# Kernel tuning notes

Hardware: AMD Instinct MI355X
Metric: run time of the kernel (lower is better)

Reference implementation:

```python
import jax, jax.numpy as jnp
import numpy as np

INPUT_SIZE = 1024
OUTPUT_SIZE = 1024
BLOCK_SIZE = 60
T = 4096
EPS = 1e-12


def setup_inputs() -> dict:
    key = jax.random.key(0)
    k1, k2, k3, k4, k5 = jax.random.split(key, 5)
    s_in = 1.0 / np.sqrt(INPUT_SIZE)
    s_out = 1.0 / np.sqrt(OUTPUT_SIZE + 2)
    return {
        "x": jax.random.normal(k1, (T, INPUT_SIZE), dtype=jnp.float32),
        "Wk": jax.random.normal(k2, (OUTPUT_SIZE, INPUT_SIZE), dtype=jnp.float32) * s_in,
        "Wq": jax.random.normal(k3, (OUTPUT_SIZE, INPUT_SIZE), dtype=jnp.float32) * s_in,
        "Wv": jax.random.normal(k4, (OUTPUT_SIZE, INPUT_SIZE), dtype=jnp.float32) * s_in,
        "Wout": jax.random.normal(k5, (INPUT_SIZE, OUTPUT_SIZE + 2), dtype=jnp.float32) * s_out,
    }


def reference(x, Wk, Wq, Wv, Wout):
    t = x.shape[0]
    # L2-normalized frame similarity / diversity  [T, T]
    x_unit = x / jnp.maximum(jnp.linalg.norm(x, axis=1, keepdims=True), EPS)
    diversity = 1.0 - x_unit @ x_unit.T

    K = x @ Wk.T
    Q = x @ Wq.T
    V = x @ Wv.T
    energies = Q @ K.T                      # [T, T]
    att_weights = jax.nn.softmax(energies, axis=-1)
    logp = jax.nn.log_softmax(energies, axis=-1)
    # normalized row entropy, then L1-normalize over T (F.normalize p=1)
    entropy = -(att_weights * logp).sum(-1) / jnp.log(jnp.float32(t))
    entropy = entropy / jnp.maximum(jnp.abs(entropy).sum(), EPS)

    # block-diagonal keep mask: same block <=> same index // block_size
    blk = jnp.arange(t) // BLOCK_SIZE
    keep = (blk[:, None] == blk[None, :]).astype(att_weights.dtype)  # [T, T]
    zero = 1.0 - keep

    att_win = att_weights * keep
    attn_rem = att_weights * zero
    div_rem = diversity * zero
    dep_factor = (div_rem * attn_rem).sum(-1) / div_rem.sum(-1)      # [T]
    # dep_factor broadcast as identical rows, masked into the kept blocks
    att_win = att_win + dep_factor[None, :] * keep

    y = att_win @ V                                                   # [T, output_size]
    characteristics = jnp.stack([entropy, dep_factor])               # [2, T] (detached in torch)
    outputs = jnp.concatenate([y, characteristics.T], axis=-1)       # [T, output_size+2]
    y_out = outputs @ Wout.T                                          # [T, input_size]
    return y_out, att_win
```

## Files before the change

### kernel.cpp

```cpp
#include <hip/hip_runtime.h>
#include <math.h>

#define T_DIM 4096
#define D_DIM 1024
#define BS 60
#define NBLK 69
#define NPART 16

typedef __attribute__((ext_vector_type(4))) float f32x4;
typedef __attribute__((ext_vector_type(8))) short short8;
#define MFMAH(a,b,c) __builtin_amdgcn_mfma_f32_16x16x32_f16((a),(b),(c),0,0,0)

static __device__ __forceinline__ ushort f2h(float f) {
  _Float16 h = (_Float16)f;
  return __builtin_bit_cast(ushort, h);
}
static __device__ __forceinline__ float h2f(ushort u) {
  _Float16 h = __builtin_bit_cast(_Float16, u);
  return (float)h;
}

__global__ __launch_bounds__(256) void k_prep(const float* __restrict__ x,
    ushort* __restrict__ xhi, ushort* __restrict__ xlo, ushort* __restrict__ u) {
  int i = blockIdx.x, tid = threadIdx.x;
  size_t off = (size_t)i * D_DIM + tid * 4;
  float4 v = *reinterpret_cast<const float4*>(x + off);
  float ss = v.x*v.x + v.y*v.y + v.z*v.z + v.w*v.w;
#pragma unroll
  for (int m = 1; m < 64; m <<= 1) ss += __shfl_xor(ss, m);
  __shared__ float sb[4];
  if ((tid & 63) == 0) sb[tid >> 6] = ss;
  __syncthreads();
  float inv = 1.0f / fmaxf(sqrtf(sb[0] + sb[1] + sb[2] + sb[3]), 1e-12f);
  ushort4 h, l, un;
  h.x = f2h(v.x); l.x = f2h(v.x - h2f(h.x)); un.x = f2h(v.x*inv);
  h.y = f2h(v.y); l.y = f2h(v.y - h2f(h.y)); un.y = f2h(v.y*inv);
  h.z = f2h(v.z); l.z = f2h(v.z - h2f(h.z)); un.z = f2h(v.z*inv);
  h.w = f2h(v.w); l.w = f2h(v.w - h2f(h.w)); un.w = f2h(v.w*inv);
  *reinterpret_cast<ushort4*>(xhi + off) = h;
  *reinterpret_cast<ushort4*>(xlo + off) = l;
  *reinterpret_cast<ushort4*>(u + off) = un;
}

__global__ __launch_bounds__(256) void k_wsplit(
    const float* __restrict__ Wq, const float* __restrict__ Wk, const float* __restrict__ Wv,
    ushort* __restrict__ Wqh, ushort* __restrict__ Wkh, ushort* __restrict__ Wvh) {
  int y = blockIdx.y;
  const float* A = (y == 0) ? Wq : (y == 1) ? Wk : Wv;
  ushort* hi = (y == 0) ? Wqh : (y == 1) ? Wkh : Wvh;
  size_t i = ((size_t)blockIdx.x * 256 + threadIdx.x) * 4;
  float4 v = *reinterpret_cast<const float4*>(A + i);
  ushort4 h;
  h.x = f2h(v.x); h.y = f2h(v.y); h.z = f2h(v.z); h.w = f2h(v.w);
  *reinterpret_cast<ushort4*>(hi + i) = h;
}

__global__ __launch_bounds__(256) void k_bsum(const ushort* __restrict__ u, float* __restrict__ Sb) {
  int b = blockIdx.x, tid = threadIdx.x;
  int j0 = b * BS;
  int w = (BS < T_DIM - j0) ? BS : (T_DIM - j0);
  int c = tid * 4;
  float4 acc = {0,0,0,0};
  for (int j = 0; j < w; ++j) {
    ushort4 v = *reinterpret_cast<const ushort4*>(u + (size_t)(j0 + j) * D_DIM + c);
    acc.x += h2f(v.x); acc.y += h2f(v.y); acc.z += h2f(v.z); acc.w += h2f(v.w);
  }
  *reinterpret_cast<float4*>(Sb + (size_t)b * D_DIM + c) = acc;
}

__global__ __launch_bounds__(256) void k_gsum(const float* __restrict__ Sb, float* __restrict__ S) {
  int c = blockIdx.x * 256 + threadIdx.x;
  float s = 0.f;
  for (int b = 0; b < NBLK; ++b) s += Sb[(size_t)b * D_DIM + c];
  S[c] = s;
}

__global__ __launch_bounds__(256,2) void k_qkv(
    const ushort* __restrict__ xhi, const ushort* __restrict__ xlo,
    const ushort* __restrict__ Wqh, const ushort* __restrict__ Wkh,
    const ushort* __restrict__ Wvh,
    ushort* __restrict__ Qhi, ushort* __restrict__ Qlo,
    ushort* __restrict__ Khi, ushort* __restrict__ Vb) {
  __shared__ __align__(16) ushort lds[28672];
  const int tid = threadIdx.x;
  const int w = tid >> 6, lane = tid & 63;
  const int wr = w >> 1, wc = w & 1;
  const int g = lane >> 4, cl = lane & 15;
  const int i0 = blockIdx.y * 128, j0 = blockIdx.x * 64;

  int adA[4], adB[2];
#pragma unroll
  for (int is = 0; is < 4; ++is) {
    int r = wr*64 + is*16 + cl;
    adA[is] = r*32 + (g ^ ((r >> 1) & 3))*8;
  }
#pragma unroll
  for (int js = 0; js < 2; ++js) {
    int r = wc*32 + js*16 + cl;
    adB[js] = r*32 + (g ^ ((r >> 1) & 3))*8;
  }
  const int ra1 = tid >> 2, ra2 = 64 + (tid >> 2), rbr = tid >> 2;
  const int sa = tid & 3;
  const int wA1 = ra1*32 + (sa ^ ((ra1 >> 1) & 3))*8;
  const int wA2 = ra2*32 + (sa ^ ((ra2 >> 1) & 3))*8;
  const int wB  = rbr*32 + (sa ^ ((rbr >> 1) & 3))*8;
  const size_t gA1 = (size_t)(i0 + ra1) * D_DIM + sa*8;
  const size_t gA2 = (size_t)(i0 + ra2) * D_DIM + sa*8;
  const size_t gB  = (size_t)(j0 + rbr) * D_DIM + sa*8;

  f32x4 accQ[4][2], accK[4][2], accV[4][2];
#pragma unroll
  for (int is = 0; is < 4; ++is)
#pragma unroll
    for (int js = 0; js < 2; ++js) {
      accQ[is][js] = (f32x4){0.f,0.f,0.f,0.f};
      accK[is][js] = (f32x4){0.f,0.f,0.f,0.f};
      accV[is][js] = (f32x4){0.f,0.f,0.f,0.f};
    }

  short8 sXh1 = *reinterpret_cast<const short8*>(xhi + gA1);
  short8 sXh2 = *reinterpret_cast<const short8*>(xhi + gA2);
  short8 sXl1 = *reinterpret_cast<const short8*>(xlo + gA1);
  short8 sXl2 = *reinterpret_cast<const short8*>(xlo + gA2);
  short8 sQh  = *reinterpret_cast<const short8*>(Wqh + gB);
  short8 sKh  = *reinterpret_cast<const short8*>(Wkh + gB);
  short8 sVh  = *reinterpret_cast<const short8*>(Wvh + gB);

  for (int ks = 0; ks < 32; ++ks) {
    const int bofs = (ks & 1) * 14336;
    *reinterpret_cast<short8*>(&lds[bofs + wA1])          = sXh1;
    *reinterpret_cast<short8*>(&lds[bofs + wA2])          = sXh2;
    *reinterpret_cast<short8*>(&lds[bofs + 4096 + wA1])   = sXl1;
    *reinterpret_cast<short8*>(&lds[bofs + 4096 + wA2])   = sXl2;
    *reinterpret_cast<short8*>(&lds[bofs + 8192 + wB])    = sQh;
    *reinterpret_cast<short8*>(&lds[bofs + 10240 + wB])   = sKh;
    *reinterpret_cast<short8*>(&lds[bofs + 12288 + wB])   = sVh;
    __syncthreads();
    short8 aH[4], aL[4], bQh[2], bKh[2], bVh[2];
#pragma unroll
    for (int is = 0; is < 4; ++is) {
      aH[is] = *reinterpret_cast<const short8*>(&lds[bofs + adA[is]]);
      aL[is] = *reinterpret_cast<const short8*>(&lds[bofs + 4096 + adA[is]]);
    }
#pragma unroll
    for (int js = 0; js < 2; ++js) {
      bQh[js] = *reinterpret_cast<const short8*>(&lds[bofs + 8192  + adB[js]]);
      bKh[js] = *reinterpret_cast<const short8*>(&lds[bofs + 10240 + adB[js]]);
      bVh[js] = *reinterpret_cast<const short8*>(&lds[bofs + 12288 + adB[js]]);
    }
    if (ks < 31) {
      const int k0 = (ks + 1) * 32;
      sXh1 = *reinterpret_cast<const short8*>(xhi + gA1 + k0);
      sXh2 = *reinterpret_cast<const short8*>(xhi + gA2 + k0);
      sXl1 = *reinterpret_cast<const short8*>(xlo + gA1 + k0);
      sXl2 = *reinterpret_cast<const short8*>(xlo + gA2 + k0);
      sQh  = *reinterpret_cast<const short8*>(Wqh + gB + k0);
      sKh  = *reinterpret_cast<const short8*>(Wkh + gB + k0);
      sVh  = *reinterpret_cast<const short8*>(Wvh + gB + k0);
    }
#pragma unroll
    for (int js = 0; js < 2; ++js)
#pragma unroll
      for (int is = 0; is < 4; ++is) {
        accQ[is][js] = MFMAH(aH[is], bQh[js], accQ[is][js]);
        accQ[is][js] = MFMAH(aL[is], bQh[js], accQ[is][js]);
        accK[is][js] = MFMAH(aH[is], bKh[js], accK[is][js]);
        accK[is][js] = MFMAH(aL[is], bKh[js], accK[is][js]);
        accV[is][js] = MFMAH(aH[is], bVh[js], accV[is][js]);
      }
  }
#pragma unroll
  for (int is = 0; is < 4; ++is)
#pragma unroll
    for (int js = 0; js < 2; ++js)
#pragma unroll
      for (int a = 0; a < 4; ++a) {
        int gi = i0 + wr*64 + is*16 + g*4 + a;
        int gj = j0 + wc*32 + js*16 + cl;
        size_t o = (size_t)gi*D_DIM + gj;
        float vq = accQ[is][js][a];
        ushort hq = f2h(vq);
        Qhi[o] = hq; Qlo[o] = f2h(vq - h2f(hq));
        Khi[o] = f2h(accK[is][js][a]);
        Vb[o]  = f2h(accV[is][js][a]);
      }
}

__global__ __launch_bounds__(256,2) void k_E(
    const ushort* __restrict__ Qhi, const ushort* __restrict__ Qlo,
    const ushort* __restrict__ Khi,
    float* __restrict__ E, float* __restrict__ pm) {
  __shared__ __align__(16) ushort lds[32768];
  __shared__ float stat_s[2][2][64];
  const int tid = threadIdx.x;
  const int bid = blockIdx.x;
  const int wg = (bid & 7) * 64 + (bid >> 3);
  const int it = wg >> 4, chunk = wg & 15;
  const int i0 = it * 128, jb = chunk * 256;
  const int w = tid >> 6, lane = tid & 63;
  const int wr = w >> 1, wc = w & 1;
  const int g = lane >> 4, cl = lane & 15;

  int adA[4], adB[8];
#pragma unroll
  for (int is = 0; is < 4; ++is) {
    int r = wr*64 + is*16 + cl;
    adA[is] = r*32 + (g ^ ((r >> 1) & 3))*8;
  }
#pragma unroll
  for (int js = 0; js < 8; ++js) {
    int r = wc*128 + js*16 + cl;
    adB[js] = 8192 + r*32 + (g ^ ((r >> 1) & 3))*8;
  }
  const int ra1 = tid >> 2, ra2 = 64 + (tid >> 2);
  const int sa = tid & 3;
  const int wA1 = ra1*32 + (sa ^ ((ra1 >> 1) & 3))*8;
  const int wA2 = ra2*32 + (sa ^ ((ra2 >> 1) & 3))*8;
  const size_t gA1 = (size_t)(i0 + ra1) * D_DIM + sa*8;
  const size_t gA2 = (size_t)(i0 + ra2) * D_DIM + sa*8;
  int wBo[4];
  size_t gBo[4];
#pragma unroll
  for (int r = 0; r < 4; ++r) {
    int rb = r*64 + (tid >> 2);
    wBo[r] = 8192 + rb*32 + (sa ^ ((rb >> 1) & 3))*8;
    gBo[r] = (size_t)(jb + rb) * D_DIM + sa*8;
  }

  f32x4 acc[4][8];
#pragma unroll
  for (int is = 0; is < 4; ++is)
#pragma unroll
    for (int js = 0; js < 8; ++js) acc[is][js] = (f32x4){0.f,0.f,0.f,0.f};

  short8 sQ1 = *reinterpret_cast<const short8*>(Qhi + gA1);
  short8 sQ2 = *reinterpret_cast<const short8*>(Qhi + gA2);
  short8 sq1 = *reinterpret_cast<const short8*>(Qlo + gA1);
  short8 sq2 = *reinterpret_cast<const short8*>(Qlo + gA2);
  short8 sK0 = *reinterpret_cast<const short8*>(Khi + gBo[0]);
  short8 sK1 = *reinterpret_cast<const short8*>(Khi + gBo[1]);
  short8 sK2 = *reinterpret_cast<const short8*>(Khi + gBo[2]);
  short8 sK3 = *reinterpret_cast<const short8*>(Khi + gBo[3]);

  for (int ks = 0; ks < 32; ++ks) {
    const int bofs = (ks & 1) * 16384;
    *reinterpret_cast<short8*>(&lds[bofs + wA1])        = sQ1;
    *reinterpret_cast<short8*>(&lds[bofs + wA2])        = sQ2;
    *reinterpret_cast<short8*>(&lds[bofs + 4096 + wA1]) = sq1;
    *reinterpret_cast<short8*>(&lds[bofs + 4096 + wA2]) = sq2;
    *reinterpret_cast<short8*>(&lds[bofs + wBo[0]])     = sK0;
    *reinterpret_cast<short8*>(&lds[bofs + wBo[1]])     = sK1;
    *reinterpret_cast<short8*>(&lds[bofs + wBo[2]])     = sK2;
    *reinterpret_cast<short8*>(&lds[bofs + wBo[3]])     = sK3;
    __syncthreads();
    short8 aQh[4], aQl[4];
#pragma unroll
    for (int is = 0; is < 4; ++is) {
      aQh[is] = *reinterpret_cast<const short8*>(&lds[bofs + adA[is]]);
      aQl[is] = *reinterpret_cast<const short8*>(&lds[bofs + 4096 + adA[is]]);
    }
    if (ks < 31) {
      const int k0 = (ks + 1) * 32;
      sQ1 = *reinterpret_cast<const short8*>(Qhi + gA1 + k0);
      sQ2 = *reinterpret_cast<const short8*>(Qhi + gA2 + k0);
      sq1 = *reinterpret_cast<const short8*>(Qlo + gA1 + k0);
      sq2 = *reinterpret_cast<const short8*>(Qlo + gA2 + k0);
      sK0 = *reinterpret_cast<const short8*>(Khi + gBo[0] + k0);
      sK1 = *reinterpret_cast<const short8*>(Khi + gBo[1] + k0);
      sK2 = *reinterpret_cast<const short8*>(Khi + gBo[2] + k0);
      sK3 = *reinterpret_cast<const short8*>(Khi + gBo[3] + k0);
    }
#pragma unroll
    for (int js = 0; js < 8; ++js) {
      short8 bK = *reinterpret_cast<const short8*>(&lds[bofs + adB[js]]);
#pragma unroll
      for (int is = 0; is < 4; ++is) {
        acc[is][js] = MFMAH(aQh[is], bK, acc[is][js]);
        acc[is][js] = MFMAH(aQl[is], bK, acc[is][js]);
      }
    }
  }
#pragma unroll
  for (int is = 0; is < 4; ++is)
#pragma unroll
    for (int a = 0; a < 4; ++a) {
      int gi = i0 + wr*64 + is*16 + g*4 + a;
      float mx = -3.0e38f;
#pragma unroll
      for (int js = 0; js < 8; ++js) {
        float e = acc[is][js][a];
        E[(size_t)gi*T_DIM + jb + wc*128 + js*16 + cl] = e;
        mx = fmaxf(mx, e);
      }
#pragma unroll
      for (int mk = 1; mk < 16; mk <<= 1) mx = fmaxf(mx, __shfl_xor(mx, mk));
      if (cl == 0) stat_s[wr][wc][is*16 + g*4 + a] = mx;
    }
  __syncthreads();
  if (tid < 128) {
    int rl = tid & 63, wr2 = tid >> 6;
    pm[(size_t)chunk*T_DIM + i0 + wr2*64 + rl] =
        fmaxf(stat_s[wr2][0][rl], stat_s[wr2][1][rl]);
  }
}

__global__ __launch_bounds__(256) void k_rowmax(const float* __restrict__ pm, float* __restrict__ mrow) {
  int i = blockIdx.x * 256 + threadIdx.x;
  float m = -3.0e38f;
  for (int c = 0; c < NPART; ++c) m = fmaxf(m, pm[(size_t)c*T_DIM + i]);
  mrow[i] = m;
}

__global__ __launch_bounds__(256,2) void k_D(
    const ushort* __restrict__ Uh, float* __restrict__ E,
    const float* __restrict__ mrow,
    float* __restrict__ eb, float* __restrict__ db,
    float* __restrict__ pZ, float* __restrict__ pWe, float* __restrict__ pWd) {
  __shared__ __align__(16) ushort lds[24576];
  __shared__ float stat_s[2][2][64][3];
  const int tid = threadIdx.x;
  const int bid = blockIdx.x;
  const int wg = (bid & 7) * 64 + (bid >> 3);
  const int it = wg >> 4, chunk = wg & 15;
  const int i0 = it * 128, jb = chunk * 256;
  const int w = tid >> 6, lane = tid & 63;
  const int wr = w >> 1, wc = w & 1;
  const int g = lane >> 4, cl = lane & 15;

  int adA[4], adB[8];
#pragma unroll
  for (int is = 0; is < 4; ++is) {
    int r = wr*64 + is*16 + cl;
    adA[is] = r*32 + (g ^ ((r >> 1) & 3))*8;
  }
#pragma unroll
  for (int js = 0; js < 8; ++js) {
    int r = wc*128 + js*16 + cl;
    adB[js] = 4096 + r*32 + (g ^ ((r >> 1) & 3))*8;
  }
  const int ra1 = tid >> 2, ra2 = 64 + (tid >> 2);
  const int sa = tid & 3;
  const int wA1 = ra1*32 + (sa ^ ((ra1 >> 1) & 3))*8;
  const int wA2 = ra2*32 + (sa ^ ((ra2 >> 1) & 3))*8;
  const size_t gA1 = (size_t)(i0 + ra1) * D_DIM + sa*8;
  const size_t gA2 = (size_t)(i0 + ra2) * D_DIM + sa*8;
  int wBo[4];
  size_t gBo[4];
#pragma unroll
  for (int r = 0; r < 4; ++r) {
    int rb = r*64 + (tid >> 2);
    wBo[r] = 4096 + rb*32 + (sa ^ ((rb >> 1) & 3))*8;
    gBo[r] = (size_t)(jb + rb) * D_DIM + sa*8;
  }

  f32x4 acc[4][8];
#pragma unroll
  for (int is = 0; is < 4; ++is)
#pragma unroll
    for (int js = 0; js < 8; ++js) acc[is][js] = (f32x4){0.f,0.f,0.f,0.f};

  short8 sU1 = *reinterpret_cast<const short8*>(Uh + gA1);
  short8 sU2 = *reinterpret_cast<const short8*>(Uh + gA2);
  short8 sV0 = *reinterpret_cast<const short8*>(Uh + gBo[0]);
  short8 sV1 = *reinterpret_cast<const short8*>(Uh + gBo[1]);
  short8 sV2 = *reinterpret_cast<const short8*>(Uh + gBo[2]);
  short8 sV3 = *reinterpret_cast<const short8*>(Uh + gBo[3]);

  for (int ks = 0; ks < 32; ++ks) {
    const int bofs = (ks & 1) * 12288;
    *reinterpret_cast<short8*>(&lds[bofs + wA1])    = sU1;
    *reinterpret_cast<short8*>(&lds[bofs + wA2])    = sU2;
    *reinterpret_cast<short8*>(&lds[bofs + wBo[0]]) = sV0;
    *reinterpret_cast<short8*>(&lds[bofs + wBo[1]]) = sV1;
    *reinterpret_cast<short8*>(&lds[bofs + wBo[2]]) = sV2;
    *reinterpret_cast<short8*>(&lds[bofs + wBo[3]]) = sV3;
    __syncthreads();
    short8 aU[4];
#pragma unroll
    for (int is = 0; is < 4; ++is)
      aU[is] = *reinterpret_cast<const short8*>(&lds[bofs + adA[is]]);
    if (ks < 31) {
      const int k0 = (ks + 1) * 32;
      sU1 = *reinterpret_cast<const short8*>(Uh + gA1 + k0);
      sU2 = *reinterpret_cast<const short8*>(Uh + gA2 + k0);
      sV0 = *reinterpret_cast<const short8*>(Uh + gBo[0] + k0);
      sV1 = *reinterpret_cast<const short8*>(Uh + gBo[1] + k0);
      sV2 = *reinterpret_cast<const short8*>(Uh + gBo[2] + k0);
      sV3 = *reinterpret_cast<const short8*>(Uh + gBo[3] + k0);
    }
#pragma unroll
    for (int js = 0; js < 8; ++js) {
      short8 bU = *reinterpret_cast<const short8*>(&lds[bofs + adB[js]]);
#pragma unroll
      for (int is = 0; is < 4; ++is)
        acc[is][js] = MFMAH(aU[is], bU, acc[is][js]);
    }
  }

  const int iw0 = i0 + wr*64;
  const int blkLo = iw0 / BS, blkHi = (iw0 + 63) / BS;
  const int jw0 = jb + wc*128;
  const bool doDiag = (jw0 < (blkHi+1)*BS) && (jw0 + 128 > blkLo*BS);

#pragma unroll
  for (int is = 0; is < 4; ++is)
#pragma unroll
    for (int a = 0; a < 4; ++a) {
      int gi = i0 + wr*64 + is*16 + g*4 + a;
      int bi = gi / BS;
      float m = mrow[gi];
      float z = 0.f, we = 0.f, wd = 0.f;
#pragma unroll
      for (int js = 0; js < 8; ++js) {
        int gj = jb + wc*128 + js*16 + cl;
        float e = E[(size_t)gi*T_DIM + gj];
        float d = acc[is][js][a];
        float p = __expf(e - m);
        z += p; we += p*e; wd += p*d;
        if (doDiag && gj / BS == bi) {
          int c = gj - bi * BS;
          eb[(size_t)gi*64 + c] = e;
          db[(size_t)gi*64 + c] = d;
        }
      }
#pragma unroll
      for (int mk = 1; mk < 16; mk <<= 1) {
        z += __shfl_xor(z, mk); we += __shfl_xor(we, mk); wd += __shfl_xor(wd, mk);
      }
      if (cl == 0) {
        int rl = is*16 + g*4 + a;
        stat_s[wr][wc][rl][0] = z;
        stat_s[wr][wc][rl][1] = we;
        stat_s[wr][wc][rl][2] = wd;
      }
    }
  __syncthreads();
  if (tid < 128) {
    int rl = tid & 63, wr2 = tid >> 6;
    size_t idx = (size_t)chunk*T_DIM + i0 + wr2*64 + rl;
    pZ[idx]  = stat_s[wr2][0][rl][0] + stat_s[wr2][1][rl][0];
    pWe[idx] = stat_s[wr2][0][rl][1] + stat_s[wr2][1][rl][1];
    pWd[idx] = stat_s[wr2][0][rl][2] + stat_s[wr2][1][rl][2];
  }
  const int zrow_ = tid >> 6;
  const int zcol  = (tid & 63) * 4;
#pragma unroll
  for (int r = 0; r < 128; r += 4)
    *reinterpret_cast<float4*>(&E[(size_t)(i0 + r + zrow_) * T_DIM + jb + zcol]) =
        (float4){0.f, 0.f, 0.f, 0.f};
}

__global__ __launch_bounds__(256) void k_merge(const float* __restrict__ pZ,
    const float* __restrict__ pWe, const float* __restrict__ pWd,
    const float* __restrict__ mrow,
    const ushort* __restrict__ Uh, const float* __restrict__ Sg, const float* __restrict__ Sb,
    const float* __restrict__ eb, const float* __restrict__ db,
    float* __restrict__ dep, float* __restrict__ ent, float* __restrict__ zrow) {
  int i = blockIdx.x, tid = threadIdx.x;
  float m = mrow[i];
  float Z = 0.f, We = 0.f, Wd = 0.f;
  for (int c = 0; c < NPART; ++c) {
    Z  += pZ [(size_t)c*T_DIM + i];
    We += pWe[(size_t)c*T_DIM + i];
    Wd += pWd[(size_t)c*T_DIM + i];
  }
  int b = i / BS, j0 = b * BS;
  int w = (BS < T_DIM - j0) ? BS : (T_DIM - j0);
  ushort4 uv = *reinterpret_cast<const ushort4*>(Uh + (size_t)i*D_DIM + tid*4);
  float4 Sv  = *reinterpret_cast<const float4*>(Sg + tid*4);
  float4 Sbv = *reinterpret_cast<const float4*>(Sb + (size_t)b*D_DIM + tid*4);
  float ux = h2f(uv.x), uy = h2f(uv.y), uz = h2f(uv.z), uw = h2f(uv.w);
  float dS  = ux*Sv.x  + uy*Sv.y  + uz*Sv.z  + uw*Sv.w;
  float dSb = ux*Sbv.x + uy*Sbv.y + uz*Sbv.z + uw*Sbv.w;
  float pb = 0.f, pdb = 0.f;
  if (tid < w) {
    float e = eb[(size_t)i*64 + tid], d = db[(size_t)i*64 + tid];
    float p = __expf(e - m);
    pb = p; pdb = p * d;
  }
  float v0 = dS, v1 = dSb, v2 = pb, v3 = pdb;
#pragma unroll
  for (int mk = 1; mk < 64; mk <<= 1) {
    v0 += __shfl_xor(v0, mk); v1 += __shfl_xor(v1, mk);
    v2 += __shfl_xor(v2, mk); v3 += __shfl_xor(v3, mk);
  }
  __shared__ float red[4][4];
  if ((tid & 63) == 0) { int wv = tid >> 6; red[0][wv]=v0; red[1][wv]=v1; red[2][wv]=v2; red[3][wv]=v3; }
  __syncthreads();
  if (tid == 0) {
    float tdS  = red[0][0]+red[0][1]+red[0][2]+red[0][3];
    float tdSb = red[1][0]+red[1][1]+red[1][2]+red[1][3];
    float s1   = red[2][0]+red[2][1]+red[2][2]+red[2][3];
    float s2   = red[3][0]+red[3][1]+red[3][2]+red[3][3];
    float invZ = 1.0f / Z;
    float num = (1.0f - s1*invZ) - (Wd - s2)*invZ;
    float den = (float)(T_DIM - w) - (tdS - tdSb);
    dep[i] = num / den;
    ent[i] = -(We*invZ - m - logf(Z)) / logf((float)T_DIM);
    zrow[i] = Z;
  }
}

__global__ __launch_bounds__(256) void k_entnorm(float* __restrict__ ent) {
  int tid = threadIdx.x;
  float s = 0.f;
  for (int i = tid; i < T_DIM; i += 256) s += fabsf(ent[i]);
#pragma unroll
  for (int mk = 1; mk < 64; mk <<= 1) s += __shfl_xor(s, mk);
  __shared__ float sb[4];
  if ((tid & 63) == 0) sb[tid >> 6] = s;
  __syncthreads();
  float inv = 1.0f / fmaxf(sb[0] + sb[1] + sb[2] + sb[3], 1e-12f);
  for (int i = tid; i < T_DIM; i += 256) ent[i] *= inv;
}

__global__ __launch_bounds__(256) void k_repack(const float* __restrict__ Wout, ushort* __restrict__ Wob) {
  int o = blockIdx.x;
  for (int k = threadIdx.x; k < 1024; k += 256)
    Wob[(size_t)o * 1024 + k] = f2h(Wout[(size_t)o * 1026 + k]);
}

__global__ __launch_bounds__(256) void k_atty(const float* __restrict__ eb, const float* __restrict__ mrow,
    const float* __restrict__ zrow, const float* __restrict__ dep, const ushort* __restrict__ Vb,
    float* __restrict__ att, ushort* __restrict__ Ybf) {
  const int b  = blockIdx.x;
  const int cc = blockIdx.y & 3, rt = blockIdx.y >> 2;
  const int j0 = b * BS;
  const int w  = (BS < T_DIM - j0) ? BS : (T_DIM - j0);
  const int r0 = rt * 12;
  __shared__ float wl[12][BS + 1];
  __shared__ __align__(16) ushort vs[BS][256];
  const int tid = threadIdx.x;
  for (int idx = tid; idx < 12 * w; idx += 256) {
    int rr = idx / w, c = idx - rr * w;
    float val = 0.f;
    if (r0 + rr < w) {
      int gi = j0 + r0 + rr;
      val = __expf(eb[(size_t)gi * 64 + c] - mrow[gi]) / zrow[gi] + dep[j0 + c];
      if (cc == 0) att[(size_t)gi * T_DIM + j0 + c] = val;
    }
    wl[rr][c] = val;
  }
  const int ccol = cc * 256;
  for (int idx = tid; idx < w * 32; idx += 256) {
    int j = idx >> 5, s = idx & 31;
    *reinterpret_cast<short8*>(&vs[j][s * 8]) =
        *reinterpret_cast<const short8*>(&Vb[(size_t)(j0 + j) * D_DIM + ccol + s * 8]);
  }
  __syncthreads();
  float acc[12];
#pragma unroll
  for (int rr = 0; rr < 12; ++rr) acc[rr] = 0.f;
  for (int j = 0; j < w; ++j) {
    float v = h2f(vs[j][tid]);
#pragma unroll
    for (int rr = 0; rr < 12; ++rr)
      acc[rr] = fmaf(wl[rr][j], v, acc[rr]);
  }
#pragma unroll
  for (int rr = 0; rr < 12; ++rr)
    if (r0 + rr < w)
      Ybf[(size_t)(j0 + r0 + rr) * D_DIM + ccol + tid] = f2h(acc[rr]);
}

__global__ __launch_bounds__(256,4) void k_final(
    const ushort* __restrict__ Ybf, const ushort* __restrict__ Wob,
    const float* __restrict__ Wout, const float* __restrict__ ent,
    const float* __restrict__ dep, float* __restrict__ yout) {
  __shared__ ushort ldsB[8192];
  const int tid = threadIdx.x;
  const int w = tid >> 6, lane = tid & 63;
  const int wr = w >> 1, wc = w & 1;
  const int g = lane >> 4, cl = lane & 15;
  const int i0 = blockIdx.y * 64, j0 = blockIdx.x * 64;
  f32x4 acc[2][2];
#pragma unroll
  for (int a = 0; a < 2; ++a)
#pragma unroll
    for (int b = 0; b < 2; ++b) acc[a][b] = (f32x4){0.f,0.f,0.f,0.f};
  const int ar0 = i0 + wr*32 + cl;

  const int r1 = tid >> 3, c1 = tid & 7;
  const int r2 = (tid + 256) >> 3, c2 = (tid + 256) & 7;
  const int lo1 = r1*64 + (c1 ^ (r1 & 7))*8;
  const int lo2 = r2*64 + (c2 ^ (r2 & 7))*8;
  const size_t gB1 = (size_t)(j0 + r1) * D_DIM + c1*8;
  const size_t gB2 = (size_t)(j0 + r2) * D_DIM + c2*8;

  short8 sB1 = *reinterpret_cast<const short8*>(Wob + gB1);
  short8 sB2 = *reinterpret_cast<const short8*>(Wob + gB2);
  short8 aY[2][2];
#pragma unroll
  for (int is = 0; is < 2; ++is)
#pragma unroll
    for (int h = 0; h < 2; ++h)
      aY[is][h] = *reinterpret_cast<const short8*>(Ybf + (size_t)(ar0 + is*16) * D_DIM + (h*4+g)*8);

  for (int ks = 0; ks < 16; ++ks) {
    const int bofs = (ks & 1) * 4096;
    *reinterpret_cast<short8*>(&ldsB[bofs + lo1]) = sB1;
    *reinterpret_cast<short8*>(&ldsB[bofs + lo2]) = sB2;
    __syncthreads();
    short8 aC[2][2];
#pragma unroll
    for (int is = 0; is < 2; ++is)
#pragma unroll
      for (int h = 0; h < 2; ++h) aC[is][h] = aY[is][h];
    if (ks < 15) {
      const int k0 = (ks + 1) * 64;
      sB1 = *reinterpret_cast<const short8*>(Wob + gB1 + k0);
      sB2 = *reinterpret_cast<const short8*>(Wob + gB2 + k0);
#pragma unroll
      for (int is = 0; is < 2; ++is)
#pragma unroll
        for (int h = 0; h < 2; ++h)
          aY[is][h] = *reinterpret_cast<const short8*>(Ybf + (size_t)(ar0 + is*16) * D_DIM + k0 + (h*4+g)*8);
    }
#pragma unroll
    for (int h = 0; h < 2; ++h)
#pragma unroll
      for (int js = 0; js < 2; ++js) {
        const int br = wc*32 + js*16 + cl;
        short8 bW = *reinterpret_cast<const short8*>(&ldsB[bofs + br*64 + ((h*4+g) ^ (br & 7))*8]);
#pragma unroll
        for (int is = 0; is < 2; ++is)
          acc[is][js] = MFMAH(aC[is][h], bW, acc[is][js]);
      }
  }
  float w1[2], w2[2];
#pragma unroll
  for (int js = 0; js < 2; ++js) {
    int gj = j0 + wc*32 + js*16 + cl;
    w1[js] = Wout[(size_t)gj * 1026 + 1024];
    w2[js] = Wout[(size_t)gj * 1026 + 1025];
  }
#pragma unroll
  for (int is = 0; is < 2; ++is)
#pragma unroll
    for (int a = 0; a < 4; ++a) {
      int gi = i0 + wr*32 + is*16 + g*4 + a;
      float e = ent[gi], d = dep[gi];
#pragma unroll
      for (int js = 0; js < 2; ++js) {
        int gj = j0 + wc*32 + js*16 + cl;
        yout[(size_t)gi * D_DIM + gj] = acc[is][js][a] + e * w1[js] + d * w2[js];
      }
    }
}

extern "C" void kernel_launch(void* const* d_in, const int* in_sizes, int n_in,
                              void* d_out, int out_size, void* d_ws, size_t ws_size,
                              hipStream_t stream) {
  const float* x    = (const float*)d_in[0];
  const float* Wk   = (const float*)d_in[1];
  const float* Wq   = (const float*)d_in[2];
  const float* Wv   = (const float*)d_in[3];
  const float* Wout = (const float*)d_in[4];
  float* out = (float*)d_out;
  char* wsb  = (char*)d_ws;

  ushort* Uh   = (ushort*)(wsb + 0);
  ushort* Vb   = (ushort*)(wsb + 8388608);
  ushort* Wqh  = (ushort*)(wsb + 16777216);
  ushort* Wkh  = (ushort*)(wsb + 18874368);
  ushort* Wvh  = (ushort*)(wsb + 20971520);
  ushort* Ybf  = (ushort*)(wsb + 23068672);
  ushort* Wob  = (ushort*)(wsb + 31457280);
  ushort* Khi  = (ushort*)(wsb + 33554432);
  ushort* xhi  = (ushort*)(wsb + 41943040);
  ushort* xlo  = (ushort*)(wsb + 50331648);
  float*  eb   = (float*)(wsb + 41943040);
  float*  db   = (float*)(wsb + 42991616);
  float*  pZ   = (float*)(wsb + 44040192);
  float*  pWe  = (float*)(wsb + 44564480);
  float*  pWd  = (float*)(wsb + 45088768);
  float*  pm   = (float*)(wsb + 45613056);
  float*  Sb   = (float*)(wsb + 46137344);
  float*  Sg   = (float*)(wsb + 46428160);
  float*  mrow = (float*)(wsb + 46432256);
  float*  zrow = (float*)(wsb + 46448640);
  float*  ent  = (float*)(wsb + 46465024);
  float*  dep  = (float*)(wsb + 46481408);

  float* yout = out;
  float* att  = out + (size_t)T_DIM * D_DIM;
  ushort* Qhi = (ushort*)yout;
  ushort* Qlo = Qhi + 4194304;
  float*  E   = att;

  k_prep<<<T_DIM, 256, 0, stream>>>(x, xhi, xlo, Uh);
  k_wsplit<<<dim3(1024, 3), 256, 0, stream>>>(Wq, Wk, Wv, Wqh, Wkh, Wvh);
  k_qkv<<<dim3(16, 32), 256, 0, stream>>>(xhi, xlo, Wqh, Wkh, Wvh,
                                          Qhi, Qlo, Khi, Vb);
  k_bsum<<<NBLK, 256, 0, stream>>>(Uh, Sb);
  k_gsum<<<4, 256, 0, stream>>>(Sb, Sg);

  k_E<<<512, 256, 0, stream>>>(Qhi, Qlo, Khi, E, pm);
  k_rowmax<<<16, 256, 0, stream>>>(pm, mrow);
  k_D<<<512, 256, 0, stream>>>(Uh, E, mrow, eb, db, pZ, pWe, pWd);
  k_merge<<<T_DIM, 256, 0, stream>>>(pZ, pWe, pWd, mrow, Uh, Sg, Sb, eb, db, dep, ent, zrow);
  k_entnorm<<<1, 256, 0, stream>>>(ent);

  k_repack<<<1024, 256, 0, stream>>>(Wout, Wob);
  k_atty<<<dim3(NBLK, 20), 256, 0, stream>>>(eb, mrow, zrow, dep, Vb, att, Ybf);
  k_final<<<dim3(16, 64), 256, 0, stream>>>(Ybf, Wob, Wout, ent, dep, yout);
}
```

Before: 293.9 us.

## Reorder diversity and energy GEMMs with int8 diversity cache and online softmax

Computes the diversity GEMM first and stores it as int8-quantized values plus fp32 diagonal blocks. The energy GEMM kernel then reads those int8 values and keeps per-tile running max, sum and weighted-sum softmax statistics. This drops the fp32 energy matrix round trip through the output buffer and the separate row-max kernel. The partial statistics are merged with rescaling in k_merge. The int8 quantization of cosine similarity adds error to the dependency factor numerator, which could hurt accuracy.

```diff
diff --git a/kernel.cpp b/kernel.cpp
--- a/kernel.cpp
+++ b/kernel.cpp
@@ -186,12 +186,122 @@
       }
 }
 
-__global__ __launch_bounds__(256,2) void k_E(
+__global__ __launch_bounds__(256,2) void k_D2(
+    const ushort* __restrict__ Uh, signed char* __restrict__ Dq,
+    float* __restrict__ db) {
+  __shared__ __align__(16) ushort lds[24576];
+  const int tid = threadIdx.x;
+  const int bid = blockIdx.x;
+  const int wg = (bid & 7) * 64 + (bid >> 3);
+  const int it = wg >> 4, chunk = wg & 15;
+  const int i0 = it * 128, jb = chunk * 256;
+  const int w = tid >> 6, lane = tid & 63;
+  const int wr = w >> 1, wc = w & 1;
+  const int g = lane >> 4, cl = lane & 15;
+
+  int adA[4], adB[8];
+#pragma unroll
+  for (int is = 0; is < 4; ++is) {
+    int r = wr*64 + is*16 + cl;
+    adA[is] = r*32 + (g ^ ((r >> 1) & 3))*8;
+  }
+#pragma unroll
+  for (int js = 0; js < 8; ++js) {
+    int r = wc*128 + js*16 + cl;
+    adB[js] = 4096 + r*32 + (g ^ ((r >> 1) & 3))*8;
+  }
+  const int ra1 = tid >> 2, ra2 = 64 + (tid >> 2);
+  const int sa = tid & 3;
+  const int wA1 = ra1*32 + (sa ^ ((ra1 >> 1) & 3))*8;
+  const int wA2 = ra2*32 + (sa ^ ((ra2 >> 1) & 3))*8;
+  const size_t gA1 = (size_t)(i0 + ra1) * D_DIM + sa*8;
+  const size_t gA2 = (size_t)(i0 + ra2) * D_DIM + sa*8;
+  int wBo[4];
+  size_t gBo[4];
+#pragma unroll
+  for (int r = 0; r < 4; ++r) {
+    int rb = r*64 + (tid >> 2);
+    wBo[r] = 4096 + rb*32 + (sa ^ ((rb >> 1) & 3))*8;
+    gBo[r] = (size_t)(jb + rb) * D_DIM + sa*8;
+  }
+
+  f32x4 acc[4][8];
+#pragma unroll
+  for (int is = 0; is < 4; ++is)
+#pragma unroll
+    for (int js = 0; js < 8; ++js) acc[is][js] = (f32x4){0.f,0.f,0.f,0.f};
+
+  short8 sU1 = *reinterpret_cast<const short8*>(Uh + gA1);
+  short8 sU2 = *reinterpret_cast<const short8*>(Uh + gA2);
+  short8 sV0 = *reinterpret_cast<const short8*>(Uh + gBo[0]);
+  short8 sV1 = *reinterpret_cast<const short8*>(Uh + gBo[1]);
+  short8 sV2 = *reinterpret_cast<const short8*>(Uh + gBo[2]);
+  short8 sV3 = *reinterpret_cast<const short8*>(Uh + gBo[3]);
+
+  for (int ks = 0; ks < 32; ++ks) {
+    const int bofs = (ks & 1) * 12288;
+    *reinterpret_cast<short8*>(&lds[bofs + wA1])    = sU1;
+    *reinterpret_cast<short8*>(&lds[bofs + wA2])    = sU2;
+    *reinterpret_cast<short8*>(&lds[bofs + wBo[0]]) = sV0;
+    *reinterpret_cast<short8*>(&lds[bofs + wBo[1]]) = sV1;
+    *reinterpret_cast<short8*>(&lds[bofs + wBo[2]]) = sV2;
+    *reinterpret_cast<short8*>(&lds[bofs + wBo[3]]) = sV3;
+    __syncthreads();
+    short8 aU[4];
+#pragma unroll
+    for (int is = 0; is < 4; ++is)
+      aU[is] = *reinterpret_cast<const short8*>(&lds[bofs + adA[is]]);
+    if (ks < 31) {
+      const int k0 = (ks + 1) * 32;
+      sU1 = *reinterpret_cast<const short8*>(Uh + gA1 + k0);
+      sU2 = *reinterpret_cast<const short8*>(Uh + gA2 + k0);
+      sV0 = *reinterpret_cast<const short8*>(Uh + gBo[0] + k0);
+      sV1 = *reinterpret_cast<const short8*>(Uh + gBo[1] + k0);
+      sV2 = *reinterpret_cast<const short8*>(Uh + gBo[2] + k0);
+      sV3 = *reinterpret_cast<const short8*>(Uh + gBo[3] + k0);
+    }
+#pragma unroll
+    for (int js = 0; js < 8; ++js) {
+      short8 bU = *reinterpret_cast<const short8*>(&lds[bofs + adB[js]]);
+#pragma unroll
+      for (int is = 0; is < 4; ++is)
+        acc[is][js] = MFMAH(aU[is], bU, acc[is][js]);
+    }
+  }
+
+  const int iw0 = i0 + wr*64;
+  const int blkLo = iw0 / BS, blkHi = (iw0 + 63) / BS;
+  const int jw0 = jb + wc*128;
+  const bool doDiag = (jw0 < (blkHi+1)*BS) && (jw0 + 128 > blkLo*BS);
+
+#pragma unroll
+  for (int is = 0; is < 4; ++is)
+#pragma unroll
+    for (int a = 0; a < 4; ++a) {
+      int gi = i0 + wr*64 + is*16 + g*4 + a;
+      int bi = gi / BS;
+#pragma unroll
+      for (int js = 0; js < 8; ++js) {
+        int gj = jb + wc*128 + js*16 + cl;
+        float d = acc[is][js][a];
+        float dc = fminf(fmaxf(d, -1.f), 1.f);
+        Dq[(size_t)gi*T_DIM + gj] = (signed char)(int)rintf(dc * 127.f);
+        if (doDiag && gj / BS == bi) {
+          int c = gj - bi * BS;
+          db[(size_t)gi*64 + c] = d;
+        }
+      }
+    }
+}
+
+__global__ __launch_bounds__(256,2) void k_E2(
     const ushort* __restrict__ Qhi, const ushort* __restrict__ Qlo,
-    const ushort* __restrict__ Khi,
-    float* __restrict__ E, float* __restrict__ pm) {
+    const ushort* __restrict__ Khi, const signed char* __restrict__ Dq,
+    float* __restrict__ att, float* __restrict__ eb,
+    float* __restrict__ pm, float* __restrict__ pZ,
+    float* __restrict__ pWe, float* __restrict__ pWd) {
   __shared__ __align__(16) ushort lds[32768];
-  __shared__ float stat_s[2][2][64];
+  __shared__ float stat_s[2][2][64][4];
   const int tid = threadIdx.x;
   const int bid = blockIdx.x;
   const int wg = (bid & 7) * 64 + (bid >> 3);
@@ -280,122 +390,6 @@
       }
     }
   }
-#pragma unroll
-  for (int is = 0; is < 4; ++is)
-#pragma unroll
-    for (int a = 0; a < 4; ++a) {
-      int gi = i0 + wr*64 + is*16 + g*4 + a;
-      float mx = -3.0e38f;
-#pragma unroll
-      for (int js = 0; js < 8; ++js) {
-        float e = acc[is][js][a];
-        E[(size_t)gi*T_DIM + jb + wc*128 + js*16 + cl] = e;
-        mx = fmaxf(mx, e);
-      }
-#pragma unroll
-      for (int mk = 1; mk < 16; mk <<= 1) mx = fmaxf(mx, __shfl_xor(mx, mk));
-      if (cl == 0) stat_s[wr][wc][is*16 + g*4 + a] = mx;
-    }
-  __syncthreads();
-  if (tid < 128) {
-    int rl = tid & 63, wr2 = tid >> 6;
-    pm[(size_t)chunk*T_DIM + i0 + wr2*64 + rl] =
-        fmaxf(stat_s[wr2][0][rl], stat_s[wr2][1][rl]);
-  }
-}
-
-__global__ __launch_bounds__(256) void k_rowmax(const float* __restrict__ pm, float* __restrict__ mrow) {
-  int i = blockIdx.x * 256 + threadIdx.x;
-  float m = -3.0e38f;
-  for (int c = 0; c < NPART; ++c) m = fmaxf(m, pm[(size_t)c*T_DIM + i]);
-  mrow[i] = m;
-}
-
-__global__ __launch_bounds__(256,2) void k_D(
-    const ushort* __restrict__ Uh, float* __restrict__ E,
-    const float* __restrict__ mrow,
-    float* __restrict__ eb, float* __restrict__ db,
-    float* __restrict__ pZ, float* __restrict__ pWe, float* __restrict__ pWd) {
-  __shared__ __align__(16) ushort lds[24576];
-  __shared__ float stat_s[2][2][64][3];
-  const int tid = threadIdx.x;
-  const int bid = blockIdx.x;
-  const int wg = (bid & 7) * 64 + (bid >> 3);
-  const int it = wg >> 4, chunk = wg & 15;
-  const int i0 = it * 128, jb = chunk * 256;
-  const int w = tid >> 6, lane = tid & 63;
-  const int wr = w >> 1, wc = w & 1;
-  const int g = lane >> 4, cl = lane & 15;
-
-  int adA[4], adB[8];
-#pragma unroll
-  for (int is = 0; is < 4; ++is) {
-    int r = wr*64 + is*16 + cl;
-    adA[is] = r*32 + (g ^ ((r >> 1) & 3))*8;
-  }
-#pragma unroll
-  for (int js = 0; js < 8; ++js) {
-    int r = wc*128 + js*16 + cl;
-    adB[js] = 4096 + r*32 + (g ^ ((r >> 1) & 3))*8;
-  }
-  const int ra1 = tid >> 2, ra2 = 64 + (tid >> 2);
-  const int sa = tid & 3;
-  const int wA1 = ra1*32 + (sa ^ ((ra1 >> 1) & 3))*8;
-  const int wA2 = ra2*32 + (sa ^ ((ra2 >> 1) & 3))*8;
-  const size_t gA1 = (size_t)(i0 + ra1) * D_DIM + sa*8;
-  const size_t gA2 = (size_t)(i0 + ra2) * D_DIM + sa*8;
-  int wBo[4];
-  size_t gBo[4];
-#pragma unroll
-  for (int r = 0; r < 4; ++r) {
-    int rb = r*64 + (tid >> 2);
-    wBo[r] = 4096 + rb*32 + (sa ^ ((rb >> 1) & 3))*8;
-    gBo[r] = (size_t)(jb + rb) * D_DIM + sa*8;
-  }
-
-  f32x4 acc[4][8];
-#pragma unroll
-  for (int is = 0; is < 4; ++is)
-#pragma unroll
-    for (int js = 0; js < 8; ++js) acc[is][js] = (f32x4){0.f,0.f,0.f,0.f};
-
-  short8 sU1 = *reinterpret_cast<const short8*>(Uh + gA1);
-  short8 sU2 = *reinterpret_cast<const short8*>(Uh + gA2);
-  short8 sV0 = *reinterpret_cast<const short8*>(Uh + gBo[0]);
-  short8 sV1 = *reinterpret_cast<const short8*>(Uh + gBo[1]);
-  short8 sV2 = *reinterpret_cast<const short8*>(Uh + gBo[2]);
-  short8 sV3 = *reinterpret_cast<const short8*>(Uh + gBo[3]);
-
-  for (int ks = 0; ks < 32; ++ks) {
-    const int bofs = (ks & 1) * 12288;
-    *reinterpret_cast<short8*>(&lds[bofs + wA1])    = sU1;
-    *reinterpret_cast<short8*>(&lds[bofs + wA2])    = sU2;
-    *reinterpret_cast<short8*>(&lds[bofs + wBo[0]]) = sV0;
-    *reinterpret_cast<short8*>(&lds[bofs + wBo[1]]) = sV1;
-    *reinterpret_cast<short8*>(&lds[bofs + wBo[2]]) = sV2;
-    *reinterpret_cast<short8*>(&lds[bofs + wBo[3]]) = sV3;
-    __syncthreads();
-    short8 aU[4];
-#pragma unroll
-    for (int is = 0; is < 4; ++is)
-      aU[is] = *reinterpret_cast<const short8*>(&lds[bofs + adA[is]]);
-    if (ks < 31) {
-      const int k0 = (ks + 1) * 32;
-      sU1 = *reinterpret_cast<const short8*>(Uh + gA1 + k0);
-      sU2 = *reinterpret_cast<const short8*>(Uh + gA2 + k0);
-      sV0 = *reinterpret_cast<const short8*>(Uh + gBo[0] + k0);
-      sV1 = *reinterpret_cast<const short8*>(Uh + gBo[1] + k0);
-      sV2 = *reinterpret_cast<const short8*>(Uh + gBo[2] + k0);
-      sV3 = *reinterpret_cast<const short8*>(Uh + gBo[3] + k0);
-    }
-#pragma unroll
-    for (int js = 0; js < 8; ++js) {
-      short8 bU = *reinterpret_cast<const short8*>(&lds[bofs + adB[js]]);
-#pragma unroll
-      for (int is = 0; is < 4; ++is)
-        acc[is][js] = MFMAH(aU[is], bU, acc[is][js]);
-    }
-  }
 
   const int iw0 = i0 + wr*64;
   const int blkLo = iw0 / BS, blkHi = (iw0 + 63) / BS;
@@ -408,20 +402,27 @@
     for (int a = 0; a < 4; ++a) {
       int gi = i0 + wr*64 + is*16 + g*4 + a;
       int bi = gi / BS;
-      float m = mrow[gi];
-      float z = 0.f, we = 0.f, wd = 0.f;
+      float ev[8], dv[8];
 #pragma unroll
       for (int js = 0; js < 8; ++js) {
         int gj = jb + wc*128 + js*16 + cl;
-        float e = E[(size_t)gi*T_DIM + gj];
-        float d = acc[is][js][a];
-        float p = __expf(e - m);
-        z += p; we += p*e; wd += p*d;
+        ev[js] = acc[is][js][a];
+        dv[js] = (float)(int)Dq[(size_t)gi*T_DIM + gj] * (1.f/127.f);
         if (doDiag && gj / BS == bi) {
           int c = gj - bi * BS;
-          eb[(size_t)gi*64 + c] = e;
-          db[(size_t)gi*64 + c] = d;
+          eb[(size_t)gi*64 + c] = ev[js];
         }
+      }
+      float tmax = ev[0];
+#pragma unroll
+      for (int js = 1; js < 8; ++js) tmax = fmaxf(tmax, ev[js]);
+#pragma unroll
+      for (int mk = 1; mk < 16; mk <<= 1) tmax = fmaxf(tmax, __shfl_xor(tmax, mk));
+      float z = 0.f, we = 0.f, wd = 0.f;
+#pragma unroll
+      for (int js = 0; js < 8; ++js) {
+        float p = __expf(ev[js] - tmax);
+        z += p; we += p * ev[js]; wd += p * dv[js];
       }
 #pragma unroll
       for (int mk = 1; mk < 16; mk <<= 1) {
@@ -429,40 +430,49 @@
       }
       if (cl == 0) {
         int rl = is*16 + g*4 + a;
-        stat_s[wr][wc][rl][0] = z;
-        stat_s[wr][wc][rl][1] = we;
-        stat_s[wr][wc][rl][2] = wd;
+        stat_s[wr][wc][rl][0] = tmax;
+        stat_s[wr][wc][rl][1] = z;
+        stat_s[wr][wc][rl][2] = we;
+        stat_s[wr][wc][rl][3] = wd;
       }
     }
   __syncthreads();
   if (tid < 128) {
     int rl = tid & 63, wr2 = tid >> 6;
+    float m0 = stat_s[wr2][0][rl][0], Z0 = stat_s[wr2][0][rl][1];
+    float We0 = stat_s[wr2][0][rl][2], Wd0 = stat_s[wr2][0][rl][3];
+    float m1 = stat_s[wr2][1][rl][0], Z1 = stat_s[wr2][1][rl][1];
+    float We1 = stat_s[wr2][1][rl][2], Wd1 = stat_s[wr2][1][rl][3];
+    float nm = fmaxf(m0, m1);
+    float s0 = __expf(m0 - nm), s1 = __expf(m1 - nm);
     size_t idx = (size_t)chunk*T_DIM + i0 + wr2*64 + rl;
-    pZ[idx]  = stat_s[wr2][0][rl][0] + stat_s[wr2][1][rl][0];
-    pWe[idx] = stat_s[wr2][0][rl][1] + stat_s[wr2][1][rl][1];
-    pWd[idx] = stat_s[wr2][0][rl][2] + stat_s[wr2][1][rl][2];
+    pm[idx]  = nm;
+    pZ[idx]  = Z0*s0 + Z1*s1;
+    pWe[idx] = We0*s0 + We1*s1;
+    pWd[idx] = Wd0*s0 + Wd1*s1;
   }
   const int zrow_ = tid >> 6;
   const int zcol  = (tid & 63) * 4;
 #pragma unroll
   for (int r = 0; r < 128; r += 4)
-    *reinterpret_cast<float4*>(&E[(size_t)(i0 + r + zrow_) * T_DIM + jb + zcol]) =
+    *reinterpret_cast<float4*>(&att[(size_t)(i0 + r + zrow_) * T_DIM + jb + zcol]) =
         (float4){0.f, 0.f, 0.f, 0.f};
 }
 
-__global__ __launch_bounds__(256) void k_merge(const float* __restrict__ pZ,
-    const float* __restrict__ pWe, const float* __restrict__ pWd,
-    const float* __restrict__ mrow,
+__global__ __launch_bounds__(256) void k_merge(const float* __restrict__ pm,
+    const float* __restrict__ pZ, const float* __restrict__ pWe, const float* __restrict__ pWd,
     const ushort* __restrict__ Uh, const float* __restrict__ Sg, const float* __restrict__ Sb,
     const float* __restrict__ eb, const float* __restrict__ db,
-    float* __restrict__ dep, float* __restrict__ ent, float* __restrict__ zrow) {
+    float* __restrict__ dep, float* __restrict__ ent,
+    float* __restrict__ mrow, float* __restrict__ zrow) {
   int i = blockIdx.x, tid = threadIdx.x;
-  float m = mrow[i];
-  float Z = 0.f, We = 0.f, Wd = 0.f;
-  for (int c = 0; c < NPART; ++c) {
-    Z  += pZ [(size_t)c*T_DIM + i];
-    We += pWe[(size_t)c*T_DIM + i];
-    Wd += pWd[(size_t)c*T_DIM + i];
+  float m = pm[i], Z = pZ[i], We = pWe[i], Wd = pWd[i];
+  for (int c = 1; c < NPART; ++c) {
+    float om = pm[(size_t)c*T_DIM + i], oZ = pZ[(size_t)c*T_DIM + i];
+    float oWe = pWe[(size_t)c*T_DIM + i], oWd = pWd[(size_t)c*T_DIM + i];
+    float nm = fmaxf(m, om);
+    float s1 = __expf(m - nm), s2 = __expf(om - nm);
+    Z = Z*s1 + oZ*s2; We = We*s1 + oWe*s2; Wd = Wd*s1 + oWd*s2; m = nm;
   }
   int b = i / BS, j0 = b * BS;
   int w = (BS < T_DIM - j0) ? BS : (T_DIM - j0);
@@ -497,7 +507,7 @@
     float den = (float)(T_DIM - w) - (tdS - tdSb);
     dep[i] = num / den;
     ent[i] = -(We*invZ - m - logf(Z)) / logf((float)T_DIM);
-    zrow[i] = Z;
+    mrow[i] = m; zrow[i] = Z;
   }
 }
 
@@ -666,6 +676,7 @@
   ushort* Wvh  = (ushort*)(wsb + 20971520);
   ushort* Ybf  = (ushort*)(wsb + 23068672);
   ushort* Wob  = (ushort*)(wsb + 31457280);
+  signed char* Dq = (signed char*)(wsb + 16777216);
   ushort* Khi  = (ushort*)(wsb + 33554432);
   ushort* xhi  = (ushort*)(wsb + 41943040);
   ushort* xlo  = (ushort*)(wsb + 50331648);
@@ -686,7 +697,6 @@
   float* att  = out + (size_t)T_DIM * D_DIM;
   ushort* Qhi = (ushort*)yout;
   ushort* Qlo = Qhi + 4194304;
-  float*  E   = att;
 
   k_prep<<<T_DIM, 256, 0, stream>>>(x, xhi, xlo, Uh);
   k_wsplit<<<dim3(1024, 3), 256, 0, stream>>>(Wq, Wk, Wv, Wqh, Wkh, Wvh);
@@ -695,10 +705,9 @@
   k_bsum<<<NBLK, 256, 0, stream>>>(Uh, Sb);
   k_gsum<<<4, 256, 0, stream>>>(Sb, Sg);
 
-  k_E<<<512, 256, 0, stream>>>(Qhi, Qlo, Khi, E, pm);
-  k_rowmax<<<16, 256, 0, stream>>>(pm, mrow);
-  k_D<<<512, 256, 0, stream>>>(Uh, E, mrow, eb, db, pZ, pWe, pWd);
-  k_merge<<<T_DIM, 256, 0, stream>>>(pZ, pWe, pWd, mrow, Uh, Sg, Sb, eb, db, dep, ent, zrow);
+  k_D2<<<512, 256, 0, stream>>>(Uh, Dq, db);
+  k_E2<<<512, 256, 0, stream>>>(Qhi, Qlo, Khi, Dq, att, eb, pm, pZ, pWe, pWd);
+  k_merge<<<T_DIM, 256, 0, stream>>>(pm, pZ, pWe, pWd, Uh, Sg, Sb, eb, db, dep, ent, mrow, zrow);
   k_entnorm<<<1, 256, 0, stream>>>(ent);
 
   k_repack<<<1024, 256, 0, stream>>>(Wout, Wob);
```

Result: slower. 310.2 us (+5.6%).
